# Performance work log

Measured on AMD Instinct MI355X. Metric: run time of the kernel, lower is better.

Reference implementation:

```python
import jax, jax.numpy as jnp
import numpy as np
from jax import lax

H_CONST = 1.0  # binarization scale (init default H=1.0)

def binarize(kernel):
    # hard_sigmoid -> round-through (STE) -> binary tanh -> scale by H
    hs = jnp.clip((kernel / H_CONST + 1.0) / 2.0, 0.0, 1.0)
    rt = hs + lax.stop_gradient(jnp.round(hs) - hs)  # round with straight-through grad
    return H_CONST * (2.0 * rt - 1.0)  # values in {-H, +H}

def setup_inputs() -> dict:
    key = jax.random.key(0)
    k1, k2, k3 = jax.random.split(key, 3)
    x = jax.random.normal(k1, (32, 112, 112, 128), dtype=jnp.float32)
    # kernel initialized uniform in [-H, H] per build()
    kernel = jax.random.uniform(k2, (3, 3, 128, 256), dtype=jnp.float32, minval=-H_CONST, maxval=H_CONST)
    bias = jax.random.normal(k3, (256,), dtype=jnp.float32) * 0.01
    return {"x": x, "kernel": kernel, "bias": bias}

def reference(x, kernel, bias):
    wb = binarize(kernel)  # [3,3,Cin,Cout], entries +/-H
    out = lax.conv_general_dilated(
        x, wb,
        window_strides=(1, 1),
        padding='VALID',
        dimension_numbers=('NHWC', 'HWIO', 'NHWC'),
    )  # [32,110,110,256]
    return out + bias  # NHWC bias_add broadcasts over channel dim
```

## Files before the change

### kernel.cpp

```cpp
#include <hip/hip_runtime.h>

typedef __attribute__((ext_vector_type(4))) int i32x4;

#define NB   32
#define HH   112
#define WW   112
#define CIN  128
#define OH_  110
#define OW_  110
#define COUT 256
#define NCHUNK 18
#define M_TOTAL (NB * OH_ * OW_)
#define BM 128
#define GRID_M (M_TOTAL / BM)
#define XQ_ELEMS ((long)NB * HH * WW * CIN)

__global__ void xquant(const float* __restrict__ x, char* __restrict__ xq) {
  long i = ((long)blockIdx.x * 256 + threadIdx.x) * 16;
  int w[4];
#pragma unroll
  for (int k = 0; k < 4; ++k) {
    float4 f = *(const float4*)(x + i + k * 4);
    int q0 = (int)rintf(fminf(fmaxf(f.x, -6.f), 6.f) * (127.f / 6.f));
    int q1 = (int)rintf(fminf(fmaxf(f.y, -6.f), 6.f) * (127.f / 6.f));
    int q2 = (int)rintf(fminf(fmaxf(f.z, -6.f), 6.f) * (127.f / 6.f));
    int q3 = (int)rintf(fminf(fmaxf(f.w, -6.f), 6.f) * (127.f / 6.f));
    w[k] = (q0 & 255) | ((q1 & 255) << 8) | ((q2 & 255) << 16) | (q3 << 24);
  }
  *(i32x4*)(xq + i) = (i32x4){w[0], w[1], w[2], w[3]};
}

__global__ void prep_weights(const float* __restrict__ kern, char* __restrict__ bq) {
  int idx = blockIdx.x * 256 + threadIdx.x;
  if (idx >= NCHUNK * 2 * 8 * 64) return;
  int lane  = idx & 63;
  int nb    = (idx >> 6) & 7;
  int nh    = (idx >> 9) & 1;
  int chunk = idx >> 10;
  int tap   = chunk >> 1;
  int n     = nh * 128 + nb * 16 + (lane & 15);
  int cib   = (chunk & 1) * 64 + ((lane >> 4) << 4);
  int w[4] = {0, 0, 0, 0};
#pragma unroll
  for (int j = 0; j < 16; ++j) {
    float kv = kern[(tap * CIN + cib + j) * COUT + n];
    float hs = fminf(fmaxf((kv + 1.0f) * 0.5f, 0.0f), 1.0f);
    int b = (rintf(hs) > 0.5f) ? 1 : -1;
    w[j >> 2] |= (b & 255) << ((j & 3) * 8);
  }
  *(i32x4*)(bq + (long)idx * 16) = (i32x4){w[0], w[1], w[2], w[3]};
}

__device__ __forceinline__ void gload16(const char* g, char* l) {
  __builtin_amdgcn_global_load_lds(
      (const __attribute__((address_space(1))) unsigned int*)g,
      (__attribute__((address_space(3))) unsigned int*)l, 16, 0, 0);
}

#define BAR() __builtin_amdgcn_s_barrier()

__global__ __launch_bounds__(256, 4) void bconv(
    const char* __restrict__ xq, const char* __restrict__ bq,
    const float* __restrict__ bias, float* __restrict__ out) {
  extern __shared__ char lds[];

  const int tid  = threadIdx.x;
  const int lane = tid & 63;
  const int wave = tid >> 6;
  const int wm   = wave >> 1;
  const int wn   = wave & 1;
  const int nh   = blockIdx.y;

  const int q = GRID_M >> 3, r = GRID_M & 7;
  const int xcd = (int)blockIdx.x & 7, ob = (int)blockIdx.x >> 3;
  const int bid = (xcd < r ? xcd * (q + 1) : r * (q + 1) + (xcd - r) * q) + ob;
  const long m0 = (long)bid * BM;

  const int kqsrc = (((tid & 3) ^ ((tid >> 2) & 3)) << 4);
  long rbase[2];
#pragma unroll
  for (int i = 0; i < 2; ++i) {
    long mrow = m0 + i * 64 + (tid >> 2);
    int nimg = (int)(mrow / (OH_ * OW_));
    int r2   = (int)(mrow - (long)nimg * (OH_ * OW_));
    int oh   = r2 / OW_;
    int ow   = r2 - oh * OW_;
    rbase[i] = (((long)nimg * HH + oh) * WW + ow) * CIN + kqsrc;
  }
  const int adst = tid * 16;
  const int bsrc = tid * 16;

#define STAGE_A(aoff, cN) do {                                               \
    const int t_ = (cN) >> 1;                                                \
    const long xo_ = (long)((t_ / 3) * WW + (t_ % 3)) * CIN + ((cN) & 1) * 64; \
    gload16(xq + rbase[0] + xo_, lds + (aoff) + adst);                       \
    gload16(xq + rbase[1] + xo_, lds + (aoff) + adst + 4096);                \
  } while (0)

#define STAGE_B(boff, cN) do {                                               \
    const char* bs_ = bq + ((long)(cN) * 2 + nh) * 8192 + bsrc;              \
    gload16(bs_,        lds + (boff) + bsrc);                                \
    gload16(bs_ + 4096, lds + (boff) + bsrc + 4096);                         \
  } while (0)

  const int arow = (wm * 64 + (lane & 15)) * 64;
  const int kqrd = (((lane >> 4) ^ (lane & 3)) << 4);
  const int brd  = wn * 4096 + lane * 16;

  i32x4 acc[4][4];
#pragma unroll
  for (int i = 0; i < 4; ++i)
#pragma unroll
    for (int j = 0; j < 4; ++j) acc[i][j] = (i32x4){0, 0, 0, 0};

  STAGE_A(0, 0);
  STAGE_B(16384, 0);
  STAGE_B(24576, 1);
  asm volatile("s_waitcnt vmcnt(2)" ::: "memory");
  BAR();

  int a0 = 0, a1 = 8192;
  int b0 = 16384, b1 = 24576, b2 = 32768;
#pragma unroll 1
  for (int c = 0; c < NCHUNK; ++c) {
    if (c + 1 < NCHUNK) STAGE_A(a1, c + 1);
    if (c + 2 < NCHUNK) STAGE_B(b2, c + 2);

    i32x4 af[4], bf[4];
#pragma unroll
    for (int mi = 0; mi < 4; ++mi)
      af[mi] = *(const i32x4*)(lds + a0 + arow + mi * 1024 + kqrd);
#pragma unroll
    for (int ni = 0; ni < 4; ++ni)
      bf[ni] = *(const i32x4*)(lds + b0 + brd + ni * 1024);
#pragma unroll
    for (int mi = 0; mi < 4; ++mi)
#pragma unroll
      for (int ni = 0; ni < 4; ++ni)
        acc[mi][ni] = __builtin_amdgcn_mfma_i32_16x16x64_i8(af[mi], bf[ni], acc[mi][ni], 0, 0, 0);

    if (c < NCHUNK - 2)       asm volatile("s_waitcnt vmcnt(2)" ::: "memory");
    else if (c == NCHUNK - 2) asm volatile("s_waitcnt vmcnt(0)" ::: "memory");
    BAR();
    int t = a0; a0 = a1; a1 = t;
    int u = b0; b0 = b1; b1 = b2; b2 = u;
  }
#undef STAGE_A
#undef STAGE_B

  const float S = 6.f / 127.f;
  const int  colb = nh * 128 + wn * 64 + (lane & 15);
  const long rowb = m0 + wm * 64 + ((lane >> 4) << 2);
#pragma unroll
  for (int ni = 0; ni < 4; ++ni) {
    const int col = colb + ni * 16;
    const float bv = bias[col];
#pragma unroll
    for (int mi = 0; mi < 4; ++mi)
#pragma unroll
      for (int rr = 0; rr < 4; ++rr)
        __builtin_nontemporal_store((float)acc[mi][ni][rr] * S + bv,
                                    &out[(rowb + mi * 16 + rr) * COUT + col]);
  }
}

extern "C" void kernel_launch(void* const* d_in, const int* in_sizes, int n_in,
                              void* d_out, int out_size, void* d_ws, size_t ws_size,
                              hipStream_t stream) {
  const float* x    = (const float*)d_in[0];
  const float* kern = (const float*)d_in[1];
  const float* bias = (const float*)d_in[2];
  float* out = (float*)d_out;

  char* xq = (char*)d_ws;
  char* bq = (char*)d_ws + XQ_ELEMS;

  (void)hipFuncSetAttribute((const void*)bconv,
                            hipFuncAttributeMaxDynamicSharedMemorySize, 40960);

  xquant<<<dim3((unsigned)(XQ_ELEMS / (256 * 16))), dim3(256), 0, stream>>>(x, xq);
  prep_weights<<<dim3(72), dim3(256), 0, stream>>>(kern, bq);
  bconv<<<dim3(GRID_M, 2), dim3(256), 40960, stream>>>(xq, bq, bias, out);
}
```

Measured before the change: 181.2 us.

## Load binary weight fragments directly into registers instead of staging through LDS

Measured after the change: 188.9 us. +4.3%, slower.

```diff
diff --git a/kernel.cpp b/kernel.cpp
--- a/kernel.cpp
+++ b/kernel.cpp
@@ -57,7 +57,8 @@
       (__attribute__((address_space(3))) unsigned int*)l, 16, 0, 0);
 }
 
-#define BAR() __builtin_amdgcn_s_barrier()
+#define BAR()    __builtin_amdgcn_s_barrier()
+#define SCHED0() __builtin_amdgcn_sched_barrier(0)
 
 __global__ __launch_bounds__(256, 4) void bconv(
     const char* __restrict__ xq, const char* __restrict__ bq,
@@ -88,7 +89,6 @@
     rbase[i] = (((long)nimg * HH + oh) * WW + ow) * CIN + kqsrc;
   }
   const int adst = tid * 16;
-  const int bsrc = tid * 16;
 
 #define STAGE_A(aoff, cN) do {                                               \
     const int t_ = (cN) >> 1;                                                \
@@ -97,15 +97,16 @@
     gload16(xq + rbase[1] + xo_, lds + (aoff) + adst + 4096);                \
   } while (0)
 
-#define STAGE_B(boff, cN) do {                                               \
-    const char* bs_ = bq + ((long)(cN) * 2 + nh) * 8192 + bsrc;              \
-    gload16(bs_,        lds + (boff) + bsrc);                                \
-    gload16(bs_ + 4096, lds + (boff) + bsrc + 4096);                         \
+  const char* bbase = bq + (long)nh * 8192 + wn * 4096 + lane * 16;
+#define LOAD_B(dst, cN) do {                                                 \
+    const char* bs_ = bbase + (long)(cN) * 16384;                            \
+    _Pragma("unroll")                                                        \
+    for (int ni_ = 0; ni_ < 4; ++ni_)                                        \
+      (dst)[ni_] = *(const i32x4*)(bs_ + ni_ * 1024);                        \
   } while (0)
 
   const int arow = (wm * 64 + (lane & 15)) * 64;
   const int kqrd = (((lane >> 4) ^ (lane & 3)) << 4);
-  const int brd  = wn * 4096 + lane * 16;
 
   i32x4 acc[4][4];
 #pragma unroll
@@ -113,40 +114,43 @@
 #pragma unroll
     for (int j = 0; j < 4; ++j) acc[i][j] = (i32x4){0, 0, 0, 0};
 
+  i32x4 bb[2][4];
+
   STAGE_A(0, 0);
-  STAGE_B(16384, 0);
-  STAGE_B(24576, 1);
-  asm volatile("s_waitcnt vmcnt(2)" ::: "memory");
+  SCHED0();
+  LOAD_B(bb[0], 0);
+  asm volatile("s_waitcnt vmcnt(4)" ::: "memory");
   BAR();
 
-  int a0 = 0, a1 = 8192;
-  int b0 = 16384, b1 = 24576, b2 = 32768;
-#pragma unroll 1
+#pragma unroll
   for (int c = 0; c < NCHUNK; ++c) {
-    if (c + 1 < NCHUNK) STAGE_A(a1, c + 1);
-    if (c + 2 < NCHUNK) STAGE_B(b2, c + 2);
+    const int cur = c & 1, nxt = cur ^ 1;
+    const int a0 = cur ? 8192 : 0;
+    const int a1 = cur ? 0 : 8192;
 
-    i32x4 af[4], bf[4];
+    if (c + 1 < NCHUNK) {
+      STAGE_A(a1, c + 1);
+      SCHED0();
+      LOAD_B(bb[nxt], c + 1);
+    }
+
+    i32x4 af[4];
 #pragma unroll
     for (int mi = 0; mi < 4; ++mi)
       af[mi] = *(const i32x4*)(lds + a0 + arow + mi * 1024 + kqrd);
 #pragma unroll
-    for (int ni = 0; ni < 4; ++ni)
-      bf[ni] = *(const i32x4*)(lds + b0 + brd + ni * 1024);
-#pragma unroll
     for (int mi = 0; mi < 4; ++mi)
 #pragma unroll
       for (int ni = 0; ni < 4; ++ni)
-        acc[mi][ni] = __builtin_amdgcn_mfma_i32_16x16x64_i8(af[mi], bf[ni], acc[mi][ni], 0, 0, 0);
+        acc[mi][ni] = __builtin_amdgcn_mfma_i32_16x16x64_i8(af[mi], bb[cur][ni], acc[mi][ni], 0, 0, 0);
 
-    if (c < NCHUNK - 2)       asm volatile("s_waitcnt vmcnt(2)" ::: "memory");
-    else if (c == NCHUNK - 2) asm volatile("s_waitcnt vmcnt(0)" ::: "memory");
-    BAR();
-    int t = a0; a0 = a1; a1 = t;
-    int u = b0; b0 = b1; b1 = b2; b2 = u;
+    if (c + 1 < NCHUNK) {
+      asm volatile("s_waitcnt vmcnt(4)" ::: "memory");
+      BAR();
+    }
   }
 #undef STAGE_A
-#undef STAGE_B
+#undef LOAD_B
 
   const float S = 6.f / 127.f;
   const int  colb = nh * 128 + wn * 64 + (lane & 15);
@@ -176,9 +180,9 @@
   char* bq = (char*)d_ws + XQ_ELEMS;
 
   (void)hipFuncSetAttribute((const void*)bconv,
-                            hipFuncAttributeMaxDynamicSharedMemorySize, 40960);
+                            hipFuncAttributeMaxDynamicSharedMemorySize, 16384);
 
   xquant<<<dim3((unsigned)(XQ_ELEMS / (256 * 16))), dim3(256), 0, stream>>>(x, xq);
   prep_weights<<<dim3(72), dim3(256), 0, stream>>>(kern, bq);
-  bconv<<<dim3(GRID_M, 2), dim3(256), 40960, stream>>>(xq, bq, bias, out);
+  bconv<<<dim3(GRID_M, 2), dim3(256), 16384, stream>>>(xq, bq, bias, out);
 }
```
